# Kernel optimization log

Hardware: AMD Instinct MI355X
Metric: run time of the kernel (lower is better)

## Reference

```python
import jax, jax.numpy as jnp
import numpy as np

NUM_HEADS = 12


def get_rel_pos(q_size, k_size, rel_pos):
    # rel_pos: (2*max(q,k)-1, C). Here q_size==k_size so no interpolation needed.
    q_coords = jnp.arange(q_size)[:, None] * max(k_size / q_size, 1.0)
    k_coords = jnp.arange(k_size)[None, :] * max(q_size / k_size, 1.0)
    rel = (q_coords - k_coords) + (k_size - 1) * max(q_size / k_size, 1.0)
    return rel_pos[rel.astype(jnp.int32)]  # (q_size, k_size, C)


def add_decomposed_rel_pos(attn, q, rel_pos_h, rel_pos_w, q_size, k_size):
    q_h, q_w = q_size
    k_h, k_w = k_size
    Rh = get_rel_pos(q_h, k_h, rel_pos_h)  # (q_h,k_h,C)
    Rw = get_rel_pos(q_w, k_w, rel_pos_w)  # (q_w,k_w,C)
    B, _, C = q.shape  # B = num_heads * batch
    r_q = q.reshape(B, q_h, q_w, C)
    rel_h = jnp.einsum('bhwc,hkc->bhwk', r_q, Rh)  # (B,q_h,q_w,k_h)
    rel_w = jnp.einsum('bhwc,wkc->bhwk', r_q, Rw)  # (B,q_h,q_w,k_w)
    attn = attn.reshape(B, q_h, q_w, k_h, k_w)
    attn = attn + rel_h[:, :, :, :, None] + rel_w[:, :, :, None, :]
    return attn.reshape(B, q_h * q_w, k_h * k_w)


def setup_inputs() -> dict:
    key = jax.random.key(0)
    ks = jax.random.split(key, 7)
    B, H, W, dim = 128, 14, 14, 768
    head_dim = dim // NUM_HEADS
    return {
        'x': jax.random.normal(ks[0], (B, H, W, dim), dtype=jnp.float32),
        'qkv_w': jax.random.normal(ks[1], (dim, 3 * dim), dtype=jnp.float32) * 0.02,
        'qkv_b': jax.random.normal(ks[2], (3 * dim,), dtype=jnp.float32) * 0.02,
        'proj_w': jax.random.normal(ks[3], (dim, dim), dtype=jnp.float32) * 0.02,
        'proj_b': jax.random.normal(ks[4], (dim,), dtype=jnp.float32) * 0.02,
        'rel_pos_h': jax.random.normal(ks[5], (2 * H - 1, head_dim), dtype=jnp.float32) * 0.02,
        'rel_pos_w': jax.random.normal(ks[6], (2 * W - 1, head_dim), dtype=jnp.float32) * 0.02,
    }


def reference(x, qkv_w, qkv_b, proj_w, proj_b, rel_pos_h, rel_pos_w):
    B, H, W, dim = x.shape
    nh = NUM_HEADS
    hd = dim // nh
    scale = hd ** -0.5
    L = H * W
    # qkv projection: (B,H,W,3*dim) -> (3, nh*B, L, hd)
    qkv = x.reshape(B, L, dim) @ qkv_w + qkv_b
    qkv = qkv.reshape(B, L, 3, nh, hd)
    qkv = jnp.transpose(qkv, (2, 3, 0, 1, 4)).reshape(3, nh * B, L, hd)
    q, k, v = qkv[0], qkv[1], qkv[2]
    attn = jnp.einsum('bqc,bkc->bqk', q * scale, k)  # (nh*B, L, L)
    attn = add_decomposed_rel_pos(attn, q, rel_pos_h, rel_pos_w, (H, W), (H, W))
    attn = jax.nn.softmax(attn, axis=-1)
    out = jnp.einsum('bqk,bkc->bqc', attn, v)  # (nh*B, L, hd)
    out = out.reshape(nh, B, H, W, hd)
    out = jnp.transpose(out, (1, 2, 3, 0, 4)).reshape(B, H, W, dim)
    return out @ proj_w + proj_b
```

## Files before the change

### kernel.cpp

```cpp
#include <hip/hip_runtime.h>
#include <stdint.h>
#include <math.h>

typedef unsigned short u16;
typedef __bf16 bf16x8 __attribute__((ext_vector_type(8)));
typedef u16 u16x8 __attribute__((ext_vector_type(8)));
typedef float f32x4 __attribute__((ext_vector_type(4)));

#define MFMA16(a,b,c) __builtin_amdgcn_mfma_f32_16x16x32_bf16((a),(b),(c),0,0,0)
#define GLOAD16(gp, lp) __builtin_amdgcn_global_load_lds( \
    (const __attribute__((address_space(1))) void*)(gp), \
    (__attribute__((address_space(3))) void*)(lp), 16, 0, 0)

__device__ __forceinline__ u16 f2bf(float f) {
  union { float f; uint32_t u; } v; v.f = f;
  return (u16)((v.u + 0x7FFFu + ((v.u >> 16) & 1u)) >> 16);
}
__device__ __forceinline__ float bits2f(uint32_t u) {
  union { uint32_t u; float f; } v; v.u = u; return v.f;
}
__device__ __forceinline__ uint32_t cvtpk(float lo, float hi) {
  uint32_t r;
  asm("v_cvt_pk_bf16_f32 %0, %1, %2" : "=v"(r) : "v"(lo), "v"(hi));
  return r;
}
__device__ __forceinline__ int4 pack8(const u16* v) {
  int4 r;
  r.x = (int)((uint32_t)v[0] | ((uint32_t)v[1] << 16));
  r.y = (int)((uint32_t)v[2] | ((uint32_t)v[3] << 16));
  r.z = (int)((uint32_t)v[4] | ((uint32_t)v[5] << 16));
  r.w = (int)((uint32_t)v[6] | ((uint32_t)v[7] << 16));
  return r;
}

__global__ void k_cvt(const float* __restrict__ in, u16* __restrict__ out, int n4, float scale) {
  int i = blockIdx.x * 256 + threadIdx.x;
  int stride = gridDim.x * 256;
  for (; i < n4; i += stride) {
    float4 v = reinterpret_cast<const float4*>(in)[i];
    ushort4 o;
    o.x = f2bf(v.x * scale); o.y = f2bf(v.y * scale);
    o.z = f2bf(v.z * scale); o.w = f2bf(v.w * scale);
    reinterpret_cast<ushort4*>(out)[i] = o;
  }
}

__global__ void k_transpose(const float* __restrict__ in, u16* __restrict__ out, int R, int C) {
  __shared__ float t[32][33];
  int tx = threadIdx.x & 31, ty = threadIdx.x >> 5;
  int c0 = blockIdx.x * 32, r0 = blockIdx.y * 32;
  #pragma unroll
  for (int i = 0; i < 4; i++)
    t[ty + i*8][tx] = in[(size_t)(r0 + ty + i*8) * C + (c0 + tx)];
  __syncthreads();
  #pragma unroll
  for (int i = 0; i < 4; i++)
    out[(size_t)(c0 + ty + i*8) * R + (r0 + tx)] = f2bf(t[tx][ty + i*8]);
}

__device__ __forceinline__ void rd_frags12(const u16* As_, const u16* Bs_, int aoff, int boff,
                                           bf16x8 (&b)[4], bf16x8 (&aA)[4], bf16x8 (&aB)[4]) {
  #pragma unroll
  for (int fc = 0; fc < 4; fc++) b[fc] = *(const bf16x8*)(Bs_ + boff + fc * 512);
  #pragma unroll
  for (int f = 0; f < 4; f++) {
    aA[f] = *(const bf16x8*)(As_ + aoff + f * 512);
    aB[f] = *(const bf16x8*)(As_ + aoff + (4 + f) * 512);
  }
}
__device__ __forceinline__ void rd_frags8(const u16* As_, const u16* Bs_, int aoff, int boff,
                                          bf16x8 (&b)[4], bf16x8 (&a)[4]) {
  #pragma unroll
  for (int fc = 0; fc < 4; fc++) b[fc] = *(const bf16x8*)(Bs_ + boff + fc * 512);
  #pragma unroll
  for (int f = 0; f < 4; f++) a[f] = *(const bf16x8*)(As_ + aoff + f * 512);
}

__global__ __launch_bounds__(512, 2) void k_qkv256(
    const u16* __restrict__ A, const u16* __restrict__ BT, const float* __restrict__ bias,
    u16* __restrict__ qo, u16* __restrict__ ko, u16* __restrict__ vo)
{
  __shared__ u16 SMEM[65536];

  int bid0 = blockIdx.x;
  int xcd = bid0 & 7, idx = bid0 >> 3;
  int base = (xcd < 2) ? xcd * 111 : 2 * 111 + (xcd - 2) * 110;
  int wgid = base + idx;
  int mt = wgid / 9, nt = wgid - (wgid / 9) * 9;

  int tid = threadIdx.x, lane = tid & 63, w = tid >> 6;
  int g = lane >> 4, c4 = lane & 15;
  int wr = w >> 2, wc = w & 3;

  int srow = lane >> 2;
  int pslot = (lane & 3) ^ ((lane >> 3) & 3);
  int cidA = w * 2;

  const u16* pA1 = A + (size_t)(mt * 256 + cidA * 16 + srow) * 768 + pslot * 8;
  const u16* pA2 = pA1 + 16 * 768;
  const u16* pB1 = BT + (size_t)(nt * 256 + cidA * 16 + srow) * 768 + pslot * 8;
  const u16* pB2 = pB1 + 16 * 768;

  int rsel = g ^ ((c4 >> 1) & 3);
  int aoff = wr * 4096 + c4 * 32 + rsel * 8;
  int boff = wc * 2048 + c4 * 32 + rsel * 8;

  f32x4 acc[8][4];
  f32x4 z4 = {0.f, 0.f, 0.f, 0.f};
  #pragma unroll
  for (int f = 0; f < 8; f++)
    #pragma unroll
    for (int fc = 0; fc < 4; fc++) acc[f][fc] = z4;

  #pragma unroll
  for (int kk = 0; kk < 3; kk++) {
    u16* dA = SMEM + kk * 8192;
    GLOAD16(pA1 + kk * 32, dA + cidA * 512);
    GLOAD16(pA2 + kk * 32, dA + (cidA + 1) * 512);
    u16* dB = SMEM + 32768 + kk * 8192;
    GLOAD16(pB1 + kk * 32, dB + cidA * 512);
    GLOAD16(pB2 + kk * 32, dB + (cidA + 1) * 512);
  }
  asm volatile("s_waitcnt vmcnt(8)" ::: "memory");
  __builtin_amdgcn_s_barrier();

  bf16x8 cb0[4], ca0[4], cd0[4], cb1[4], ca1[4], cd1[4];
  rd_frags12(SMEM, SMEM + 32768, aoff, boff, cb0, ca0, cd0);
  {
    u16* dA = SMEM + 3 * 8192;
    GLOAD16(pA1 + 3 * 32, dA + cidA * 512);
    GLOAD16(pA2 + 3 * 32, dA + (cidA + 1) * 512);
    u16* dB = SMEM + 32768 + 3 * 8192;
    GLOAD16(pB1 + 3 * 32, dB + cidA * 512);
    GLOAD16(pB2 + 3 * 32, dB + (cidA + 1) * 512);
  }
  asm volatile("s_waitcnt vmcnt(6)" ::: "memory");

#define QKV_REGION(K, CB, CAA, CAB, NB, NAA, NAB)                           \
  __builtin_amdgcn_s_barrier();                                             \
  if ((K) < 20) {                                                           \
    u16* dA_ = SMEM + (((K) + 4) & 3) * 8192;                               \
    GLOAD16(pA1 + ((K) + 4) * 32, dA_ + cidA * 512);                        \
    GLOAD16(pA2 + ((K) + 4) * 32, dA_ + (cidA + 1) * 512);                  \
    u16* dB_ = SMEM + 32768 + (((K) + 4) & 3) * 8192;                       \
    GLOAD16(pB1 + ((K) + 4) * 32, dB_ + cidA * 512);                        \
    GLOAD16(pB2 + ((K) + 4) * 32, dB_ + (cidA + 1) * 512);                  \
  }                                                                         \
  __builtin_amdgcn_s_setprio(1);                                            \
  _Pragma("unroll") for (int f_ = 0; f_ < 4; f_++)                          \
    _Pragma("unroll") for (int fc_ = 0; fc_ < 4; fc_++)                     \
      acc[f_][fc_] = MFMA16(CAA[f_], CB[fc_], acc[f_][fc_]);                \
  if ((K) < 23)                                                             \
    rd_frags12(SMEM + (((K) + 1) & 3) * 8192,                               \
               SMEM + 32768 + (((K) + 1) & 3) * 8192, aoff, boff,           \
               NB, NAA, NAB);                                               \
  _Pragma("unroll") for (int f_ = 0; f_ < 4; f_++)                          \
    _Pragma("unroll") for (int fc_ = 0; fc_ < 4; fc_++)                     \
      acc[4 + f_][fc_] = MFMA16(CAB[f_], CB[fc_], acc[4 + f_][fc_]);        \
  __builtin_amdgcn_s_setprio(0);                                            \
  if ((K) < 20)       { asm volatile("s_waitcnt vmcnt(6)" ::: "memory"); }  \
  else if ((K) == 20) { asm volatile("s_waitcnt vmcnt(2)" ::: "memory"); }  \
  else if ((K) == 21) { asm volatile("s_waitcnt vmcnt(0)" ::: "memory"); }

  for (int kk = 0; kk < 24; kk += 2) {
    QKV_REGION(kk,     cb0, ca0, cd0, cb1, ca1, cd1)
    QKV_REGION(kk + 1, cb1, ca1, cd1, cb0, ca0, cd0)
  }
#undef QKV_REGION

  int i3 = nt / 3;
  u16* dst = (i3 == 0) ? qo : (i3 == 1) ? ko : vo;
  int head = (nt - i3 * 3) * 4 + wc;
  float bsv[4];
  #pragma unroll
  for (int fc = 0; fc < 4; fc++) bsv[fc] = bias[nt * 256 + wc * 64 + fc * 16 + c4];

  int mbase = mt * 256 + wr * 128 + g * 4;
  #pragma unroll
  for (int f = 0; f < 8; f++) {
    #pragma unroll
    for (int j = 0; j < 4; j++) {
      int mm = mbase + f * 16 + j;
      int bb2 = mm / 196, ll = mm - bb2 * 196;
      size_t ro = (size_t)((head * 128 + bb2) * 196 + ll) * 64;
      #pragma unroll
      for (int fc = 0; fc < 4; fc++)
        dst[ro + fc * 16 + c4] = f2bf(acc[f][fc][j] + bsv[fc]);
    }
  }
}

__global__ __launch_bounds__(256, 2) void k_proj256(
    const u16* __restrict__ A, const u16* __restrict__ BT, const float* __restrict__ bias,
    float* __restrict__ out)
{
  __shared__ u16 SMEM[32768];

  int bid0 = blockIdx.x;
  int bid = (bid0 & 7) * 147 + (bid0 >> 3);
  int nt = bid % 6, mt = bid / 6;

  int tid = threadIdx.x, lane = tid & 63, w = tid >> 6;
  int g = lane >> 4, c4 = lane & 15;
  int wr = w >> 1, wc = w & 1;

  int srow = lane >> 2;
  int pslot = (lane & 3) ^ ((lane >> 3) & 3);
  int cidA = w * 2;

  const u16* pA1 = A + (size_t)(mt * 128 + cidA * 16 + srow) * 768 + pslot * 8;
  const u16* pA2 = pA1 + 16 * 768;
  const u16* pB1 = BT + (size_t)(nt * 128 + cidA * 16 + srow) * 768 + pslot * 8;
  const u16* pB2 = pB1 + 16 * 768;

  int rsel = g ^ ((c4 >> 1) & 3);
  int aoff = wr * 2048 + c4 * 32 + rsel * 8;
  int boff = wc * 2048 + c4 * 32 + rsel * 8;

  f32x4 acc[4][4];
  f32x4 z4 = {0.f, 0.f, 0.f, 0.f};
  #pragma unroll
  for (int f = 0; f < 4; f++)
    #pragma unroll
    for (int fc = 0; fc < 4; fc++) acc[f][fc] = z4;

  #pragma unroll
  for (int kk = 0; kk < 3; kk++) {
    u16* dA = SMEM + kk * 4096;
    GLOAD16(pA1 + kk * 32, dA + cidA * 512);
    GLOAD16(pA2 + kk * 32, dA + (cidA + 1) * 512);
    u16* dB = SMEM + 16384 + kk * 4096;
    GLOAD16(pB1 + kk * 32, dB + cidA * 512);
    GLOAD16(pB2 + kk * 32, dB + (cidA + 1) * 512);
  }
  asm volatile("s_waitcnt vmcnt(8)" ::: "memory");
  __builtin_amdgcn_s_barrier();

  bf16x8 cbE[4], caE[4], cbO[4], caO[4];
  rd_frags8(SMEM, SMEM + 16384, aoff, boff, cbE, caE);
  {
    u16* dA = SMEM + 3 * 4096;
    GLOAD16(pA1 + 3 * 32, dA + cidA * 512);
    GLOAD16(pA2 + 3 * 32, dA + (cidA + 1) * 512);
    u16* dB = SMEM + 16384 + 3 * 4096;
    GLOAD16(pB1 + 3 * 32, dB + cidA * 512);
    GLOAD16(pB2 + 3 * 32, dB + (cidA + 1) * 512);
  }
  asm volatile("s_waitcnt vmcnt(6)" ::: "memory");

#define PROJ_REGION(K, CB, CA, NB, NA)                                      \
  __builtin_amdgcn_s_barrier();                                             \
  if ((K) < 20) {                                                           \
    u16* dA_ = SMEM + (((K) + 4) & 3) * 4096;                               \
    GLOAD16(pA1 + ((K) + 4) * 32, dA_ + cidA * 512);                        \
    GLOAD16(pA2 + ((K) + 4) * 32, dA_ + (cidA + 1) * 512);                  \
    u16* dB_ = SMEM + 16384 + (((K) + 4) & 3) * 4096;                       \
    GLOAD16(pB1 + ((K) + 4) * 32, dB_ + cidA * 512);                        \
    GLOAD16(pB2 + ((K) + 4) * 32, dB_ + (cidA + 1) * 512);                  \
  }                                                                         \
  __builtin_amdgcn_s_setprio(1);                                            \
  _Pragma("unroll") for (int f_ = 0; f_ < 4; f_++)                          \
    _Pragma("unroll") for (int fc_ = 0; fc_ < 4; fc_++)                     \
      acc[f_][fc_] = MFMA16(CA[f_], CB[fc_], acc[f_][fc_]);                 \
  if ((K) < 23)                                                             \
    rd_frags8(SMEM + (((K) + 1) & 3) * 4096,                                \
              SMEM + 16384 + (((K) + 1) & 3) * 4096, aoff, boff, NB, NA);   \
  __builtin_amdgcn_s_setprio(0);                                            \
  if ((K) < 20)       { asm volatile("s_waitcnt vmcnt(6)" ::: "memory"); }  \
  else if ((K) == 20) { asm volatile("s_waitcnt vmcnt(2)" ::: "memory"); }  \
  else if ((K) == 21) { asm volatile("s_waitcnt vmcnt(0)" ::: "memory"); }

  for (int kk = 0; kk < 24; kk += 2) {
    PROJ_REGION(kk,     cbE, caE, cbO, caO)
    PROJ_REGION(kk + 1, cbO, caO, cbE, caE)
  }
#undef PROJ_REGION

  #pragma unroll
  for (int fc = 0; fc < 4; fc++) {
    int n0 = nt * 128 + wc * 64 + fc * 16 + c4;
    float bs = bias[n0];
    #pragma unroll
    for (int fr = 0; fr < 4; fr++)
      #pragma unroll
      for (int j = 0; j < 4; j++) {
        int m = mt * 128 + wr * 64 + fr * 16 + g * 4 + j;
        out[(size_t)m * 768 + n0] = acc[fr][fc][j] + bs;
      }
  }
}

#define VP 232
__global__ __launch_bounds__(256, 2) void k_attn(
    const u16* __restrict__ Q, const u16* __restrict__ Kg, const u16* __restrict__ Vg,
    const u16* __restrict__ RPH, const u16* __restrict__ RPW, u16* __restrict__ Ows)
{
  __shared__ u16 K64[208 * 64];
  __shared__ u16 Krel[208 * 40];
  __shared__ u16 VT[64 * VP];
  __shared__ u16 Qrel[4][16 * 40];

  int bh = blockIdx.x;
  int hh = bh >> 7, bb = bh & 127;
  int tid = threadIdx.x, lane = tid & 63, w = tid >> 6;
  int g = lane >> 4, c4 = lane & 15;

  const u16* kbase = Kg + (size_t)bh * 12544;
  const u16* vbase = Vg + (size_t)bh * 12544;
  const u16* qbase = Q + (size_t)bh * 12544;

  const float KSC = 0.18033688011f;
  for (int ch = tid; ch < 1664; ch += 256) {
    int row = ch >> 3, s = ch & 7;
    u16 outv[8];
    if (row < 196) {
      u16x8 v = *(const u16x8*)(kbase + row * 64 + s * 8);
      #pragma unroll
      for (int e = 0; e < 8; e++)
        outv[e] = f2bf(bits2f((uint32_t)v[e] << 16) * KSC);
    } else {
      #pragma unroll
      for (int e = 0; e < 8; e++) outv[e] = 0;
    }
    *(int4*)(K64 + row * 64 + ((s ^ (row & 7)) * 8)) = pack8(outv);
  }
  if (tid < 208) {
    int k = tid;
    int kh = k / 14, kw2 = k - kh * 14;
    #pragma unroll
    for (int s = 0; s < 5; s++) {
      u16 vals[8];
      #pragma unroll
      for (int e = 0; e < 8; e++) {
        int c = s * 8 + e;
        u16 x = 0;
        if (k < 196) {
          if (c == kh) x = 0x3F80;
          else if (c == 14 + kw2) x = 0x3F80;
        } else {
          if (c == 28) x = 0x3F80;
        }
        vals[e] = x;
      }
      *(int4*)(Krel + k * 40 + s * 8) = pack8(vals);
    }
  }
  for (int i = tid; i < 2048; i += 256) {
    int chn = i >> 5, c = 192 + (i & 31);
    if (c >= 196 && c < VP) VT[chn * VP + c] = 0;
  }
  for (int ch2 = tid; ch2 < 784; ch2 += 256) {
    int kp = ch2 % 98, cb = ch2 / 98;
    int key = kp * 2, cz = cb * 8;
    u16x8 a = *(const u16x8*)(vbase + key * 64 + cz);
    u16x8 b2 = *(const u16x8*)(vbase + (key + 1) * 64 + cz);
    int kk = key & 31;
    int colp = (key >> 5) * 32 + ((kk & 15) >> 2) * 8 + (kk & 3) + ((kk >> 4) << 2);
    #pragma unroll
    for (int j = 0; j < 8; j++) {
      uint32_t pk = (uint32_t)a[j] | ((uint32_t)b2[j] << 16);
      *(uint32_t*)(VT + (cz + j) * VP + colp) = pk;
    }
  }
  __syncthreads();

  int t1 = 16 + c4; if (t1 > 26) t1 = 26;
  bf16x8 rh00 = *(const bf16x8*)(RPH + c4 * 64 + g * 8);
  bf16x8 rh01 = *(const bf16x8*)(RPH + c4 * 64 + 32 + g * 8);
  bf16x8 rh10 = *(const bf16x8*)(RPH + t1 * 64 + g * 8);
  bf16x8 rh11 = *(const bf16x8*)(RPH + t1 * 64 + 32 + g * 8);
  bf16x8 rw00 = *(const bf16x8*)(RPW + c4 * 64 + g * 8);
  bf16x8 rw01 = *(const bf16x8*)(RPW + c4 * 64 + 32 + g * 8);
  bf16x8 rw10 = *(const bf16x8*)(RPW + t1 * 64 + g * 8);
  bf16x8 rw11 = *(const bf16x8*)(RPW + t1 * 64 + 32 + g * 8);

  f32x4 z4 = {0.f, 0.f, 0.f, 0.f};

  int qi0 = w * 16 + c4;
  int qr0 = qi0 > 195 ? 195 : qi0;
  bf16x8 qa0 = *(const bf16x8*)(qbase + qr0 * 64 + g * 8);
  bf16x8 qa1 = *(const bf16x8*)(qbase + qr0 * 64 + 32 + g * 8);

  for (int qt = w; qt < 13; qt += 4) {
    int qi = qt * 16 + c4;
    bf16x8 nq0, nq1;
    int qn = qt + 4;
    if (qn < 13) {
      int qrn = qn * 16 + c4; if (qrn > 195) qrn = 195;
      nq0 = *(const bf16x8*)(qbase + qrn * 64 + g * 8);
      nq1 = *(const bf16x8*)(qbase + qrn * 64 + 32 + g * 8);
    }

    u16* Qr = (u16*)Qrel[w];
    {
      int4 zz = {0, 0, 0, 0};
      *(int4*)(Qr + lane * 8) = zz;
      if (lane < 16) *(int4*)(Qr + 512 + lane * 8) = zz;
      if (g == 0) Qr[c4 * 40 + 28] = f2bf(-30000.f);
    }

    int qh = qi / 14;
    int qwv = qi - qh * 14;

    f32x4 e0 = MFMA16(rh00, qa0, z4); e0 = MFMA16(rh01, qa1, e0);
    f32x4 e1 = MFMA16(rh10, qa0, z4); e1 = MFMA16(rh11, qa1, e1);
    #pragma unroll
    for (int tt = 0; tt < 2; tt++) {
      f32x4 e = tt ? e1 : e0;
      #pragma unroll
      for (int j = 0; j < 4; j++) {
        int t = tt * 16 + 4 * g + j;
        int kh = qh + 13 - t;
        if ((unsigned)kh <= 13u) Qr[c4 * 40 + kh] = f2bf(e[j]);
      }
    }
    f32x4 f0 = MFMA16(rw00, qa0, z4); f0 = MFMA16(rw01, qa1, f0);
    f32x4 f1 = MFMA16(rw10, qa0, z4); f1 = MFMA16(rw11, qa1, f1);
    #pragma unroll
    for (int tt = 0; tt < 2; tt++) {
      f32x4 e = tt ? f1 : f0;
      #pragma unroll
      for (int j = 0; j < 4; j++) {
        int t = tt * 16 + 4 * g + j;
        int kw3 = qwv + 13 - t;
        if ((unsigned)kw3 <= 13u) Qr[c4 * 40 + 14 + kw3] = f2bf(e[j]);
      }
    }

    bf16x8 qrelB = *(const bf16x8*)(Qr + c4 * 40 + g * 8);

    f32x4 St[13];
    #pragma unroll
    for (int i = 0; i < 13; i++) {
      int key = i * 16 + c4;
      const u16* kr = K64 + key * 64;
      int sw = key & 7;
      bf16x8 kb0 = *(const bf16x8*)(kr + ((g ^ sw) * 8));
      bf16x8 kb1 = *(const bf16x8*)(kr + (((4 + g) ^ sw) * 8));
      f32x4 acc = MFMA16(kb0, qa0, z4);
      acc = MFMA16(kb1, qa1, acc);
      bf16x8 krl = *(const bf16x8*)(Krel + key * 40 + g * 8);
      St[i] = MFMA16(krl, qrelB, acc);
    }

    float mx = -3.0e38f;
    #pragma unroll
    for (int i = 0; i < 13; i++)
      #pragma unroll
      for (int j = 0; j < 4; j++) mx = fmaxf(mx, St[i][j]);
    mx = fmaxf(mx, __shfl_xor(mx, 16));
    mx = fmaxf(mx, __shfl_xor(mx, 32));

    float ls = 0.f;
    f32x4 O[4] = {z4, z4, z4, z4};
    #pragma unroll
    for (int p = 0; p < 7; p++) {
      float pe[8];
      #pragma unroll
      for (int j2 = 0; j2 < 4; j2++) { pe[j2] = exp2f(St[2 * p][j2] - mx); ls += pe[j2]; }
      if (p < 6) {
        #pragma unroll
        for (int j2 = 0; j2 < 4; j2++) { pe[4 + j2] = exp2f(St[2 * p + 1][j2] - mx); ls += pe[4 + j2]; }
      } else {
        #pragma unroll
        for (int j2 = 0; j2 < 4; j2++) pe[4 + j2] = 0.f;
      }
      union { uint32_t u[4]; bf16x8 v; } pb;
      pb.u[0] = cvtpk(pe[0], pe[1]);
      pb.u[1] = cvtpk(pe[2], pe[3]);
      pb.u[2] = cvtpk(pe[4], pe[5]);
      pb.u[3] = cvtpk(pe[6], pe[7]);
      #pragma unroll
      for (int ct = 0; ct < 4; ct++) {
        bf16x8 va = *(const bf16x8*)(VT + (ct * 16 + c4) * VP + p * 32 + g * 8);
        O[ct] = MFMA16(va, pb.v, O[ct]);
      }
    }
    ls += __shfl_xor(ls, 16);
    ls += __shfl_xor(ls, 32);

    if (qi < 196) {
      float inv = 1.f / ls;
      size_t obase = (size_t)(bb * 196 + qi) * 768 + hh * 64;
      #pragma unroll
      for (int ct = 0; ct < 4; ct++) {
        uint32_t o0 = cvtpk(O[ct][0] * inv, O[ct][1] * inv);
        uint32_t o1 = cvtpk(O[ct][2] * inv, O[ct][3] * inv);
        uint2 ov = {o0, o1};
        *(uint2*)(Ows + obase + ct * 16 + g * 4) = ov;
      }
    }
    qa0 = nq0; qa1 = nq1;
  }
}

extern "C" void kernel_launch(void* const* d_in, const int* in_sizes, int n_in,
                              void* d_out, int out_size, void* d_ws, size_t ws_size,
                              hipStream_t stream) {
  (void)in_sizes; (void)n_in; (void)out_size; (void)ws_size;
  const float* x      = (const float*)d_in[0];
  const float* qkv_w  = (const float*)d_in[1];
  const float* qkv_b  = (const float*)d_in[2];
  const float* proj_w = (const float*)d_in[3];
  const float* proj_b = (const float*)d_in[4];
  const float* rph    = (const float*)d_in[5];
  const float* rpw    = (const float*)d_in[6];
  float* out = (float*)d_out;
  char* ws = (char*)d_ws;

  u16* xb   = (u16*)(ws);
  u16* wT   = (u16*)(ws + 38535168);
  u16* pT   = (u16*)(ws + 42074112);
  u16* rphb = (u16*)(ws + 43253760);
  u16* rpwb = (u16*)(ws + 43257856);
  u16* qws  = (u16*)(ws + 43261952);
  u16* kws  = (u16*)(ws + 81797120);
  u16* vws  = (u16*)(ws + 120332288);
  u16* Ows  = xb;

  const float LOG2E = 1.44269504f;
  k_cvt<<<2048, 256, 0, stream>>>(x, xb, 4816896, 1.0f);
  k_cvt<<<2, 256, 0, stream>>>(rph, rphb, 432, LOG2E);
  k_cvt<<<2, 256, 0, stream>>>(rpw, rpwb, 432, LOG2E);
  k_transpose<<<dim3(72, 24), 256, 0, stream>>>(qkv_w, wT, 768, 2304);
  k_transpose<<<dim3(24, 24), 256, 0, stream>>>(proj_w, pT, 768, 768);
  k_qkv256<<<882, 512, 0, stream>>>(xb, wT, qkv_b, qws, kws, vws);
  k_attn<<<1536, 256, 0, stream>>>(qws, kws, vws, rphb, rpwb, Ows);
  k_proj256<<<1176, 256, 0, stream>>>(Ows, pT, proj_b, out);
}
```

Measured before the change: 270.2 us.

## Shrink GEMM pipelines to double-buffered LDS to raise occupancy

Both the QKV and output-projection GEMM kernels drop from a four-stage LDS ring with register-level fragment prefetch to a two-stage double buffer that reads fragments, barriers, issues the next loads, then computes. Shared memory is halved and launch bounds request four blocks per CU instead of two, aiming for more resident waves to hide latency. In exchange, latency hiding within a block drops, an extra barrier per k-step is added, and the tighter launch bounds may restrict registers for the large accumulator tiles, risking spills.

Result: slower. 1.045 ms, median of 2 (+286.6%).

```diff
diff --git a/kernel.cpp b/kernel.cpp
--- a/kernel.cpp
+++ b/kernel.cpp
@@ -76,11 +76,11 @@
   for (int f = 0; f < 4; f++) a[f] = *(const bf16x8*)(As_ + aoff + f * 512);
 }
 
-__global__ __launch_bounds__(512, 2) void k_qkv256(
+__global__ __launch_bounds__(512, 4) void k_qkv256(
     const u16* __restrict__ A, const u16* __restrict__ BT, const float* __restrict__ bias,
     u16* __restrict__ qo, u16* __restrict__ ko, u16* __restrict__ vo)
 {
-  __shared__ u16 SMEM[65536];
+  __shared__ u16 SMEM[32768];
 
   int bid0 = blockIdx.x;
   int xcd = bid0 & 7, idx = bid0 >> 3;
@@ -113,60 +113,51 @@
     for (int fc = 0; fc < 4; fc++) acc[f][fc] = z4;
 
   #pragma unroll
-  for (int kk = 0; kk < 3; kk++) {
+  for (int kk = 0; kk < 2; kk++) {
     u16* dA = SMEM + kk * 8192;
     GLOAD16(pA1 + kk * 32, dA + cidA * 512);
     GLOAD16(pA2 + kk * 32, dA + (cidA + 1) * 512);
-    u16* dB = SMEM + 32768 + kk * 8192;
+    u16* dB = SMEM + 16384 + kk * 8192;
     GLOAD16(pB1 + kk * 32, dB + cidA * 512);
     GLOAD16(pB2 + kk * 32, dB + (cidA + 1) * 512);
   }
-  asm volatile("s_waitcnt vmcnt(8)" ::: "memory");
+  asm volatile("s_waitcnt vmcnt(4)" ::: "memory");
   __builtin_amdgcn_s_barrier();
 
-  bf16x8 cb0[4], ca0[4], cd0[4], cb1[4], ca1[4], cd1[4];
-  rd_frags12(SMEM, SMEM + 32768, aoff, boff, cb0, ca0, cd0);
-  {
-    u16* dA = SMEM + 3 * 8192;
-    GLOAD16(pA1 + 3 * 32, dA + cidA * 512);
-    GLOAD16(pA2 + 3 * 32, dA + (cidA + 1) * 512);
-    u16* dB = SMEM + 32768 + 3 * 8192;
-    GLOAD16(pB1 + 3 * 32, dB + cidA * 512);
-    GLOAD16(pB2 + 3 * 32, dB + (cidA + 1) * 512);
-  }
-  asm volatile("s_waitcnt vmcnt(6)" ::: "memory");
-
-#define QKV_REGION(K, CB, CAA, CAB, NB, NAA, NAB)                           \
-  __builtin_amdgcn_s_barrier();                                             \
-  if ((K) < 20) {                                                           \
-    u16* dA_ = SMEM + (((K) + 4) & 3) * 8192;                               \
-    GLOAD16(pA1 + ((K) + 4) * 32, dA_ + cidA * 512);                        \
-    GLOAD16(pA2 + ((K) + 4) * 32, dA_ + (cidA + 1) * 512);                  \
-    u16* dB_ = SMEM + 32768 + (((K) + 4) & 3) * 8192;                       \
-    GLOAD16(pB1 + ((K) + 4) * 32, dB_ + cidA * 512);                        \
-    GLOAD16(pB2 + ((K) + 4) * 32, dB_ + (cidA + 1) * 512);                  \
-  }                                                                         \
-  __builtin_amdgcn_s_setprio(1);                                            \
-  _Pragma("unroll") for (int f_ = 0; f_ < 4; f_++)                          \
-    _Pragma("unroll") for (int fc_ = 0; fc_ < 4; fc_++)                     \
-      acc[f_][fc_] = MFMA16(CAA[f_], CB[fc_], acc[f_][fc_]);                \
-  if ((K) < 23)                                                             \
-    rd_frags12(SMEM + (((K) + 1) & 3) * 8192,                               \
-               SMEM + 32768 + (((K) + 1) & 3) * 8192, aoff, boff,           \
-               NB, NAA, NAB);                                               \
-  _Pragma("unroll") for (int f_ = 0; f_ < 4; f_++)                          \
-    _Pragma("unroll") for (int fc_ = 0; fc_ < 4; fc_++)                     \
-      acc[4 + f_][fc_] = MFMA16(CAB[f_], CB[fc_], acc[4 + f_][fc_]);        \
-  __builtin_amdgcn_s_setprio(0);                                            \
-  if ((K) < 20)       { asm volatile("s_waitcnt vmcnt(6)" ::: "memory"); }  \
-  else if ((K) == 20) { asm volatile("s_waitcnt vmcnt(2)" ::: "memory"); }  \
-  else if ((K) == 21) { asm volatile("s_waitcnt vmcnt(0)" ::: "memory"); }
+#define QKV_BODY(K, S)                                                      \
+  {                                                                         \
+    const u16* As_ = SMEM + (S) * 8192;                                     \
+    const u16* Bs_ = SMEM + 16384 + (S) * 8192;                             \
+    bf16x8 bfr[4], afrA[4], afrB[4];                                        \
+    rd_frags12(As_, Bs_, aoff, boff, bfr, afrA, afrB);                      \
+    asm volatile("s_waitcnt lgkmcnt(0)" ::: "memory");                      \
+    __builtin_amdgcn_s_barrier();                \
+    if ((K) < 22) {                                                         \
+      u16* dA_ = SMEM + (S) * 8192;                                         \
+      GLOAD16(pA1 + ((K) + 2) * 32, dA_ + cidA * 512);                      \
+      GLOAD16(pA2 + ((K) + 2) * 32, dA_ + (cidA + 1) * 512);                \
+      u16* dB_ = SMEM + 16384 + (S) * 8192;                                 \
+      GLOAD16(pB1 + ((K) + 2) * 32, dB_ + cidA * 512);                      \
+      GLOAD16(pB2 + ((K) + 2) * 32, dB_ + (cidA + 1) * 512);                \
+    }                                                                       \
+    __builtin_amdgcn_s_setprio(1);                                          \
+    _Pragma("unroll") for (int f_ = 0; f_ < 4; f_++)                        \
+      _Pragma("unroll") for (int fc_ = 0; fc_ < 4; fc_++)                   \
+        acc[f_][fc_] = MFMA16(afrA[f_], bfr[fc_], acc[f_][fc_]);            \
+    _Pragma("unroll") for (int f_ = 0; f_ < 4; f_++)                        \
+      _Pragma("unroll") for (int fc_ = 0; fc_ < 4; fc_++)                   \
+        acc[4 + f_][fc_] = MFMA16(afrB[f_], bfr[fc_], acc[4 + f_][fc_]);    \
+    __builtin_amdgcn_s_setprio(0);                                          \
+    if ((K) < 22)       { asm volatile("s_waitcnt vmcnt(4)" ::: "memory"); }\
+    else if ((K) == 22) { asm volatile("s_waitcnt vmcnt(0)" ::: "memory"); }\
+    __builtin_amdgcn_s_barrier();                     \
+  }
 
   for (int kk = 0; kk < 24; kk += 2) {
-    QKV_REGION(kk,     cb0, ca0, cd0, cb1, ca1, cd1)
-    QKV_REGION(kk + 1, cb1, ca1, cd1, cb0, ca0, cd0)
-  }
-#undef QKV_REGION
+    QKV_BODY(kk, 0)
+    QKV_BODY(kk + 1, 1)
+  }
+#undef QKV_BODY
 
   int i3 = nt / 3;
   u16* dst = (i3 == 0) ? qo : (i3 == 1) ? ko : vo;
@@ -190,11 +181,11 @@
   }
 }
 
-__global__ __launch_bounds__(256, 2) void k_proj256(
+__global__ __launch_bounds__(256, 4) void k_proj256(
     const u16* __restrict__ A, const u16* __restrict__ BT, const float* __restrict__ bias,
     float* __restrict__ out)
 {
-  __shared__ u16 SMEM[32768];
+  __shared__ u16 SMEM[16384];
 
   int bid0 = blockIdx.x;
   int bid = (bid0 & 7) * 147 + (bid0 >> 3);
@@ -225,56 +216,48 @@
     for (int fc = 0; fc < 4; fc++) acc[f][fc] = z4;
 
   #pragma unroll
-  for (int kk = 0; kk < 3; kk++) {
+  for (int kk = 0; kk < 2; kk++) {
     u16* dA = SMEM + kk * 4096;
     GLOAD16(pA1 + kk * 32, dA + cidA * 512);
     GLOAD16(pA2 + kk * 32, dA + (cidA + 1) * 512);
-    u16* dB = SMEM + 16384 + kk * 4096;
+    u16* dB = SMEM + 8192 + kk * 4096;
     GLOAD16(pB1 + kk * 32, dB + cidA * 512);
     GLOAD16(pB2 + kk * 32, dB + (cidA + 1) * 512);
   }
-  asm volatile("s_waitcnt vmcnt(8)" ::: "memory");
+  asm volatile("s_waitcnt vmcnt(4)" ::: "memory");
   __builtin_amdgcn_s_barrier();
 
-  bf16x8 cbE[4], caE[4], cbO[4], caO[4];
-  rd_frags8(SMEM, SMEM + 16384, aoff, boff, cbE, caE);
-  {
-    u16* dA = SMEM + 3 * 4096;
-    GLOAD16(pA1 + 3 * 32, dA + cidA * 512);
-    GLOAD16(pA2 + 3 * 32, dA + (cidA + 1) * 512);
-    u16* dB = SMEM + 16384 + 3 * 4096;
-    GLOAD16(pB1 + 3 * 32, dB + cidA * 512);
-    GLOAD16(pB2 + 3 * 32, dB + (cidA + 1) * 512);
-  }
-  asm volatile("s_waitcnt vmcnt(6)" ::: "memory");
-
-#define PROJ_REGION(K, CB, CA, NB, NA)                                      \
-  __builtin_amdgcn_s_barrier();                                             \
-  if ((K) < 20) {                                                           \
-    u16* dA_ = SMEM + (((K) + 4) & 3) * 4096;                               \
-    GLOAD16(pA1 + ((K) + 4) * 32, dA_ + cidA * 512);                        \
-    GLOAD16(pA2 + ((K) + 4) * 32, dA_ + (cidA + 1) * 512);                  \
-    u16* dB_ = SMEM + 16384 + (((K) + 4) & 3) * 4096;                       \
-    GLOAD16(pB1 + ((K) + 4) * 32, dB_ + cidA * 512);                        \
-    GLOAD16(pB2 + ((K) + 4) * 32, dB_ + (cidA + 1) * 512);                  \
-  }                                                                         \
-  __builtin_amdgcn_s_setprio(1);                                            \
-  _Pragma("unroll") for (int f_ = 0; f_ < 4; f_++)                          \
-    _Pragma("unroll") for (int fc_ = 0; fc_ < 4; fc_++)                     \
-      acc[f_][fc_] = MFMA16(CA[f_], CB[fc_], acc[f_][fc_]);                 \
-  if ((K) < 23)                                                             \
-    rd_frags8(SMEM + (((K) + 1) & 3) * 4096,                                \
-              SMEM + 16384 + (((K) + 1) & 3) * 4096, aoff, boff, NB, NA);   \
-  __builtin_amdgcn_s_setprio(0);                                            \
-  if ((K) < 20)       { asm volatile("s_waitcnt vmcnt(6)" ::: "memory"); }  \
-  else if ((K) == 20) { asm volatile("s_waitcnt vmcnt(2)" ::: "memory"); }  \
-  else if ((K) == 21) { asm volatile("s_waitcnt vmcnt(0)" ::: "memory"); }
+#define PROJ_BODY(K, S)                                                     \
+  {                                                                         \
+    const u16* As_ = SMEM + (S) * 4096;                                     \
+    const u16* Bs_ = SMEM + 8192 + (S) * 4096;                              \
+    bf16x8 bfr[4], afr[4];                                                  \
+    rd_frags8(As_, Bs_, aoff, boff, bfr, afr);                              \
+    asm volatile("s_waitcnt lgkmcnt(0)" ::: "memory");                      \
+    __builtin_amdgcn_s_barrier();                                           \
+    if ((K) < 22) {                                                         \
+      u16* dA_ = SMEM + (S) * 4096;                                         \
+      GLOAD16(pA1 + ((K) + 2) * 32, dA_ + cidA * 512);                      \
+      GLOAD16(pA2 + ((K) + 2) * 32, dA_ + (cidA + 1) * 512);                \
+      u16* dB_ = SMEM + 8192 + (S) * 4096;                                  \
+      GLOAD16(pB1 + ((K) + 2) * 32, dB_ + cidA * 512);                      \
+      GLOAD16(pB2 + ((K) + 2) * 32, dB_ + (cidA + 1) * 512);                \
+    }                                                                       \
+    __builtin_amdgcn_s_setprio(1);                                          \
+    _Pragma("unroll") for (int f_ = 0; f_ < 4; f_++)                        \
+      _Pragma("unroll") for (int fc_ = 0; fc_ < 4; fc_++)                   \
+        acc[f_][fc_] = MFMA16(afr[f_], bfr[fc_], acc[f_][fc_]);             \
+    __builtin_amdgcn_s_setprio(0);                                          \
+    if ((K) < 22)       { asm volatile("s_waitcnt vmcnt(4)" ::: "memory"); }\
+    else if ((K) == 22) { asm volatile("s_waitcnt vmcnt(0)" ::: "memory"); }\
+    __builtin_amdgcn_s_barrier();                                           \
+  }
 
   for (int kk = 0; kk < 24; kk += 2) {
-    PROJ_REGION(kk,     cbE, caE, cbO, caO)
-    PROJ_REGION(kk + 1, cbO, caO, cbE, caE)
-  }
-#undef PROJ_REGION
+    PROJ_BODY(kk, 0)
+    PROJ_BODY(kk + 1, 1)
+  }
+#undef PROJ_BODY
 
   #pragma unroll
   for (int fc = 0; fc < 4; fc++) {
```
